# Kernel tuning notes

Hardware: AMD Instinct MI355X
Metric: run time of the kernel (lower is better)

## Reference

```python
import jax, jax.numpy as jnp
import numpy as np
from jax import lax


def setup_inputs() -> dict:
    key = jax.random.key(0)
    ks = jax.random.split(key, 4)
    B, Cin, H, W = 8, 64, 128, 128
    Cout, kh, kw = 64, 3, 3
    K = kh * kw
    x = jax.random.normal(ks[0], (B, Cin, H, W), jnp.float32)
    # small init so predicted offsets stay in a sensible range
    w_offset = jax.random.normal(ks[1], (2 * K, Cin, kh, kw), jnp.float32) * 0.01
    b_offset = jnp.zeros((2 * K,), jnp.float32)
    w_conv = jax.random.normal(ks[2], (Cout, Cin, kh, kw), jnp.float32) * (1.0 / np.sqrt(Cin * K))
    b_conv = jax.random.normal(ks[3], (Cout,), jnp.float32) * 0.01
    return dict(x=x, w_offset=w_offset, b_offset=b_offset, w_conv=w_conv, b_conv=b_conv)


def _deform_conv2d(x, offset, w, b, stride=(1, 1), padding=(1, 1), dilation=(1, 1)):
    B, Cin, Hin, Win = x.shape
    Cout, _, kh, kw = w.shape
    K = kh * kw
    sh, sw = stride; ph, pw = padding; dh, dw = dilation
    Hout = (Hin + 2 * ph - dh * (kh - 1) - 1) // sh + 1
    Wout = (Win + 2 * pw - dw * (kw - 1) - 1) // sw + 1
    # torchvision layout: [B, K, (dy,dx), Hout, Wout]
    off = offset.reshape(B, K, 2, Hout, Wout)
    dy, dx = off[:, :, 0], off[:, :, 1]
    hs = jnp.arange(Hout, dtype=x.dtype) * sh - ph          # [Hout]
    ws = jnp.arange(Wout, dtype=x.dtype) * sw - pw          # [Wout]
    ky = jnp.repeat(jnp.arange(kh, dtype=x.dtype) * dh, kw)  # [K]
    kx = jnp.tile(jnp.arange(kw, dtype=x.dtype) * dw, kh)    # [K]
    py = dy + (ky[:, None, None] + hs[None, :, None])[None]  # [B,K,Hout,Wout]
    px = dx + (kx[:, None, None] + ws[None, None, :])[None]

    def sample(img, py, px):
        y0 = jnp.floor(py); x0 = jnp.floor(px)
        wy1 = py - y0; wx1 = px - x0
        wy0 = 1.0 - wy1; wx0 = 1.0 - wx1

        def gather(yy, xx, wgt):
            valid = (yy >= 0) & (yy <= Hin - 1) & (xx >= 0) & (xx <= Win - 1)
            yi = jnp.clip(yy, 0, Hin - 1).astype(jnp.int32)
            xi = jnp.clip(xx, 0, Win - 1).astype(jnp.int32)
            vals = img[:, yi, xi]  # [Cin,K,Hout,Wout]
            return vals * (wgt * valid)[None]

        return (gather(y0, x0, wy0 * wx0) + gather(y0, x0 + 1, wy0 * wx1)
                + gather(y0 + 1, x0, wy1 * wx0) + gather(y0 + 1, x0 + 1, wy1 * wx1))

    sampled = jax.vmap(sample)(x, py, px)  # [B,Cin,K,Hout,Wout]
    out = jnp.einsum('bckhw,ock->bohw', sampled, w.reshape(Cout, Cin, K))
    return out + b[None, :, None, None]


def reference(x, w_offset, b_offset, w_conv, b_conv):
    # offset-predicting conv (stride 1, same padding, dilation 1)
    offset = lax.conv_general_dilated(
        x, w_offset, window_strides=(1, 1), padding=[(1, 1), (1, 1)],
        rhs_dilation=(1, 1), dimension_numbers=('NCHW', 'OIHW', 'NCHW'))
    offset = offset + b_offset[None, :, None, None]
    # deformable conv v1 (mask is None in _get_deformation)
    return _deform_conv2d(x, offset, w_conv, b_conv)
```

## Files before the change

### kernel.cpp

```cpp
#include <hip/hip_runtime.h>
#include <stdint.h>

#define H 128
#define W 128
#define CIN 64
#define COUT 64
#define NB 8
#define WR 4
#define WC 16
#define CW 20
#define PLANE 162

typedef __attribute__((ext_vector_type(4))) float f32x4;
typedef __attribute__((ext_vector_type(2))) _Float16 f16x2;
typedef __attribute__((ext_vector_type(8))) _Float16 f16x8;
typedef __attribute__((ext_vector_type(4))) unsigned int u32x4;
typedef __attribute__((ext_vector_type(2))) unsigned int u32x2;

__device__ __forceinline__ f16x2 bch2(unsigned u) { return __builtin_bit_cast(f16x2, u); }
__device__ __forceinline__ unsigned bcu(f16x2 v) { return __builtin_bit_cast(unsigned, v); }

__global__ __launch_bounds__(256) void x_to_nhwc(const float* __restrict__ x,
                                                 _Float16* __restrict__ xt) {
    __shared__ _Float16 tile[W][68];
    int bh = blockIdx.x;
    int h = bh & (H - 1), b = bh >> 7;
    int t = threadIdx.x;
    #pragma unroll
    for (int i = 0; i < 8; ++i) {
        int idx = i * 256 + t;
        int c = idx >> 5;
        int w4 = (idx & 31) << 2;
        f32x4 v = *(const f32x4*)(x + (((size_t)(b * CIN + c) * H + h) * W + w4));
        #pragma unroll
        for (int j = 0; j < 4; ++j) tile[w4 + j][c] = (_Float16)v[j];
    }
    __syncthreads();
    _Float16* dst = xt + (size_t)bh * W * CIN;
    #pragma unroll
    for (int i = 0; i < 8; ++i) {
        int idx = i * 256 + t;
        int w = idx >> 4;
        int c4 = (idx & 15) << 2;
        *(uint2*)(dst + (size_t)w * CIN + c4) = *(const uint2*)&tile[w][c4];
    }
}

__global__ __launch_bounds__(256) void prep_w(const float* __restrict__ wo,
                                              const float* __restrict__ wc,
                                              _Float16* __restrict__ wao2,
                                              _Float16* __restrict__ wac2) {
    int t = blockIdx.x * 256 + threadIdx.x;
    if (t < 18432) {
        int j = t & 7, l = (t >> 3) & 63, m = (t >> 9) & 1, kk = t >> 10;
        int cout = m * 16 + (l & 15);
        int cin = (kk & 1) * 32 + ((l >> 4) << 3) + j;
        wao2[t] = (cout < 18) ? (_Float16)wo[(cout * 64 + cin) * 9 + (kk >> 1)]
                              : (_Float16)0.f;
    } else if (t < 18432 + 36864) {
        int u = t - 18432;
        int j = u & 7, l = (u >> 3) & 63, m = (u >> 9) & 3, kk = u >> 11;
        int cout = m * 16 + (l & 15);
        int cin = (kk & 1) * 32 + ((l >> 4) << 3) + j;
        wac2[u] = (_Float16)wc[(cout * 64 + cin) * 9 + (kk >> 1)];
    }
}

__global__ __launch_bounds__(256, 4) void deform_fused(const _Float16* __restrict__ xt,
                                                       const _Float16* __restrict__ wao2,
                                                       const _Float16* __restrict__ wac2,
                                                       const float* __restrict__ bo,
                                                       const float* __restrict__ bconv,
                                                       float* __restrict__ out) {
    __shared__ u32x4   s_x[8 * PLANE];
    __shared__ unsigned s_aw[4][9][16];
    __shared__ u32x2   s_wq[4][9][16];

    int bid = blockIdx.x;
    int b = bid & 7;
    int r = bid >> 3;
    int h0 = ((r >> 3) & 31) << 2;
    int w0 = (r & 7) << 4;

    int r_lo = max(0, h0 - 2), r_hi = min(H - 1, h0 + 5);
    int c_lo = max(0, w0 - 2), c_hi = min(W - 1, w0 + WC + 1);
    int nr = r_hi - r_lo + 1, nc = c_hi - c_lo + 1;

    int t = threadIdx.x;
    int lane = t & 63, wv = t >> 6;
    int pcol = lane & 15, hq = lane >> 4;
    int h = h0 + wv;
    int wp = w0 + pcol;

    const _Float16* xb = xt + (size_t)b * H * W * CIN;

    {
        int cs = t >> 3, ch = t & 7;
        bool act = t < nc * 8;
        for (int rr = 0; rr < nr; ++rr) {
            if (act) {
                u32x4 v = *(const u32x4*)(xb + (size_t)((r_lo + rr) * W + c_lo + cs) * CIN + (ch << 3));
                s_x[ch * PLANE + rr * CW + cs] = v;
            }
        }
    }
    __syncthreads();

    f32x4 ao0 = {}, ao1 = {};
    #pragma unroll
    for (int k = 0; k < 9; ++k) {
        int yy = h + k / 3 - 1;
        int xx = wp + k % 3 - 1;
        bool valid = ((unsigned)yy < (unsigned)H) && ((unsigned)xx < (unsigned)W);
        int yc = min(max(yy, 0), H - 1);
        int xc = min(max(xx, 0), W - 1);
        int s = (yc - r_lo) * CW + (xc - c_lo);
        u32x4 ve = s_x[hq * PLANE + s];
        u32x4 vo = s_x[(4 + hq) * PLANE + s];
        u32x4 z = {};
        if (!valid) { ve = z; vo = z; }
        f16x8 be = __builtin_bit_cast(f16x8, ve);
        f16x8 bod = __builtin_bit_cast(f16x8, vo);
        const _Float16* wb = wao2 + (size_t)(4 * k) * 512 + lane * 8;
        ao0 = __builtin_amdgcn_mfma_f32_16x16x32_f16(*(const f16x8*)(wb), be, ao0, 0, 0, 0);
        ao1 = __builtin_amdgcn_mfma_f32_16x16x32_f16(*(const f16x8*)(wb + 512), be, ao1, 0, 0, 0);
        ao0 = __builtin_amdgcn_mfma_f32_16x16x32_f16(*(const f16x8*)(wb + 1024), bod, ao0, 0, 0, 0);
        ao1 = __builtin_amdgcn_mfma_f32_16x16x32_f16(*(const f16x8*)(wb + 1536), bod, ao1, 0, 0, 0);
    }

    auto setup = [&](int k, float dy, float dx) {
        float py = (float)(h + k / 3 - 1) + dy;
        float px = (float)(wp + k % 3 - 1) + dx;
        float y0f = floorf(py), x0f = floorf(px);
        float fy = py - y0f, fx = px - x0f;
        float vy0 = (y0f >= 0.f  && y0f <= 127.f) ? 1.f : 0.f;
        float vy1 = (y0f >= -1.f && y0f <= 126.f) ? 1.f : 0.f;
        float vx0 = (x0f >= 0.f  && x0f <= 127.f) ? 1.f : 0.f;
        float vx1 = (x0f >= -1.f && x0f <= 126.f) ? 1.f : 0.f;
        float g0 = (1.f - fy) * (1.f - fx) * vy0 * vx0;
        float g1 = (1.f - fy) * fx         * vy0 * vx1;
        float g2 = fy * (1.f - fx)         * vy1 * vx0;
        float g3 = fy * fx                 * vy1 * vx1;
        int y0i = (int)fminf(fmaxf(y0f, 0.f), 127.f);
        int x0i = (int)fminf(fmaxf(x0f, 0.f), 127.f);
        int y1i = (int)fminf(fmaxf(y0f + 1.f, 0.f), 127.f);
        int x1i = (int)fminf(fmaxf(x0f + 1.f, 0.f), 127.f);
        unsigned dxb = (unsigned)(x1i - x0i);
        unsigned dyb = (unsigned)(y1i - y0i);
        bool inw = (y0i >= r_lo) && (y1i <= r_hi) && (x0i >= c_lo) && (x1i <= c_hi);
        unsigned s00 = inw ? (unsigned)((y0i - r_lo) * CW + (x0i - c_lo)) : 0u;
        unsigned a00 = (unsigned)(y0i * W + x0i);
        s_aw[wv][k][pcol] = s00 | (dxb << 9) | (dyb << 10) | (inw ? 0u : (1u << 11)) | (a00 << 12);
        u32x2 wq;
        wq[0] = bcu((f16x2){(_Float16)g0, (_Float16)g1});
        wq[1] = bcu((f16x2){(_Float16)g2, (_Float16)g3});
        s_wq[wv][k][pcol] = wq;
    };
    f32x4 bo4 = *(const f32x4*)(bo + 4 * hq);
    setup(2 * hq,     ao0[0] + bo4[0], ao0[1] + bo4[1]);
    setup(2 * hq + 1, ao0[2] + bo4[2], ao0[3] + bo4[3]);
    if (hq == 0) setup(8, ao1[0] + bo[16], ao1[1] + bo[17]);
    __syncthreads();

    const _Float16* xh = xb + (hq << 3);
    const u32x4* se = s_x + hq * PLANE;
    const u32x4* so = s_x + (4 + hq) * PLANE;
    f32x4 acc[4] = {};

    unsigned AW[9];
    u32x2   WQ[9];
    #pragma unroll
    for (int k = 0; k < 9; ++k) {
        AW[k] = s_aw[wv][k][pcol];
        WQ[k] = s_wq[wv][k][pcol];
    }

    u32x4 E[2][4], O[2][4];
    #define FETCH(kk, buf)                                                    \
        {                                                                     \
            unsigned aw_ = AW[kk];                                            \
            unsigned s00_ = aw_ & 511u;                                       \
            unsigned dx_ = (aw_ >> 9) & 1u;                                   \
            unsigned dy_ = (aw_ >> 10) & 1u;                                  \
            unsigned s01_ = s00_ + dx_, s10_ = s00_ + dy_ * CW, s11_ = s10_ + dx_; \
            E[buf][0] = se[s00_]; E[buf][1] = se[s01_];                       \
            E[buf][2] = se[s10_]; E[buf][3] = se[s11_];                       \
            O[buf][0] = so[s00_]; O[buf][1] = so[s01_];                       \
            O[buf][2] = so[s10_]; O[buf][3] = so[s11_];                       \
            asm volatile("" : "+v"(E[buf][0]), "+v"(E[buf][1]),               \
                              "+v"(E[buf][2]), "+v"(E[buf][3]),               \
                              "+v"(O[buf][0]), "+v"(O[buf][1]),               \
                              "+v"(O[buf][2]), "+v"(O[buf][3]));              \
        }

    FETCH(0, 0);
    #pragma unroll
    for (int k = 0; k < 9; ++k) {
        const int cur = k & 1, nxt = cur ^ 1;
        if (k < 8) FETCH(k + 1, nxt);
        unsigned aw = AW[k];
        u32x2 wq = WQ[k];
        u32x4 e00 = E[cur][0], e01 = E[cur][1], e10 = E[cur][2], e11 = E[cur][3];
        u32x4 o00 = O[cur][0], o01 = O[cur][1], o10 = O[cur][2], o11 = O[cur][3];
        if (__builtin_expect((aw & (1u << 11)) != 0u, 0)) {
            unsigned dxb = (aw >> 9) & 1u;
            unsigned dyb = (aw >> 10) & 1u;
            unsigned a00 = aw >> 12;
            unsigned a01 = a00 + dxb;
            unsigned a10 = a00 + (dyb << 7);
            unsigned a11 = a10 + dxb;
            const _Float16* p00 = xh + (size_t)a00 * CIN;
            const _Float16* p01 = xh + (size_t)a01 * CIN;
            const _Float16* p10 = xh + (size_t)a10 * CIN;
            const _Float16* p11 = xh + (size_t)a11 * CIN;
            e00 = *(const u32x4*)p00; o00 = *(const u32x4*)(p00 + 32);
            e01 = *(const u32x4*)p01; o01 = *(const u32x4*)(p01 + 32);
            e10 = *(const u32x4*)p10; o10 = *(const u32x4*)(p10 + 32);
            e11 = *(const u32x4*)p11; o11 = *(const u32x4*)(p11 + 32);
        }
        f16x2 wab = bch2(wq[0]);
        f16x2 wcd = bch2(wq[1]);
        f16x2 w00d = (f16x2){wab[0], wab[0]};
        f16x2 w01d = (f16x2){wab[1], wab[1]};
        f16x2 w10d = (f16x2){wcd[0], wcd[0]};
        f16x2 w11d = (f16x2){wcd[1], wcd[1]};
        u32x4 fe, fo;
        #pragma unroll
        for (int d = 0; d < 4; ++d) {
            f16x2 ve = bch2(e00[d]) * w00d + bch2(e01[d]) * w01d
                     + bch2(e10[d]) * w10d + bch2(e11[d]) * w11d;
            f16x2 vo = bch2(o00[d]) * w00d + bch2(o01[d]) * w01d
                     + bch2(o10[d]) * w10d + bch2(o11[d]) * w11d;
            fe[d] = bcu(ve);
            fo[d] = bcu(vo);
        }
        f16x8 bfe = __builtin_bit_cast(f16x8, fe);
        f16x8 bfo = __builtin_bit_cast(f16x8, fo);
        const _Float16* ab = wac2 + (size_t)(8 * k) * 512 + lane * 8;
        #pragma unroll
        for (int m = 0; m < 4; ++m)
            acc[m] = __builtin_amdgcn_mfma_f32_16x16x32_f16(*(const f16x8*)(ab + m * 512), bfe, acc[m], 0, 0, 0);
        #pragma unroll
        for (int m = 0; m < 4; ++m)
            acc[m] = __builtin_amdgcn_mfma_f32_16x16x32_f16(*(const f16x8*)(ab + (4 + m) * 512), bfo, acc[m], 0, 0, 0);
    }
    #undef FETCH

    #pragma unroll
    for (int m = 0; m < 4; ++m) {
        f32x4 bc4 = *(const f32x4*)(bconv + m * 16 + (hq << 2));
        #pragma unroll
        for (int r2 = 0; r2 < 4; ++r2) {
            int co = (m << 4) + (hq << 2) + r2;
            out[(((size_t)b * COUT + co) * H + h) * W + wp] = acc[m][r2] + bc4[r2];
        }
    }
}

extern "C" void kernel_launch(void* const* d_in, const int* in_sizes, int n_in,
                              void* d_out, int out_size, void* d_ws, size_t ws_size,
                              hipStream_t stream) {
    const float* x  = (const float*)d_in[0];
    const float* wo = (const float*)d_in[1];
    const float* bo = (const float*)d_in[2];
    const float* wc = (const float*)d_in[3];
    const float* bc = (const float*)d_in[4];
    float* out = (float*)d_out;

    _Float16* xt   = (_Float16*)d_ws;
    _Float16* wao2 = (_Float16*)((char*)d_ws + (size_t)NB * H * W * CIN * 2);
    _Float16* wac2 = wao2 + 18432;

    x_to_nhwc<<<NB * H, 256, 0, stream>>>(x, xt);
    prep_w<<<(18432 + 36864 + 255) / 256, 256, 0, stream>>>(wo, wc, wao2, wac2);
    deform_fused<<<NB * H * W / (WR * WC), 256, 0, stream>>>(xt, wao2, wac2, bo, bc, out);
}
```

Before: 56.74 us.

## Split input channels across two wave halves with shared-memory reduction

Doubles the block to 512 threads. Each pair of waves splits the 64 input channels: one half handles the first 32 channels and the other the last 32, for both the offset conv and the deformable sampling plus MFMA. Partial offset sums and final accumulators are combined through shared memory with extra barriers. This halves per-thread registers and bilinear work to raise parallelism and occupancy, at the cost of duplicated offset setup reads, two reductions and more synchronisation.

```diff
diff --git a/kernel.cpp b/kernel.cpp
--- a/kernel.cpp
+++ b/kernel.cpp
@@ -10,6 +10,7 @@
 #define WC 16
 #define CW 20
 #define PLANE 162
+#define REDS 260
 
 typedef __attribute__((ext_vector_type(4))) float f32x4;
 typedef __attribute__((ext_vector_type(2))) _Float16 f16x2;
@@ -66,15 +67,14 @@
     }
 }
 
-__global__ __launch_bounds__(256, 4) void deform_fused(const _Float16* __restrict__ xt,
+__global__ __launch_bounds__(512, 5) void deform_fused(const _Float16* __restrict__ xt,
                                                        const _Float16* __restrict__ wao2,
                                                        const _Float16* __restrict__ wac2,
                                                        const float* __restrict__ bo,
                                                        const float* __restrict__ bconv,
                                                        float* __restrict__ out) {
-    __shared__ u32x4   s_x[8 * PLANE];
-    __shared__ unsigned s_aw[4][9][16];
-    __shared__ u32x2   s_wq[4][9][16];
+    __shared__ u32x4 s_x[8 * PLANE];
+    __shared__ float s_meta[4][432];
 
     int bid = blockIdx.x;
     int b = bid & 7;
@@ -88,8 +88,11 @@
 
     int t = threadIdx.x;
     int lane = t & 63, wv = t >> 6;
+    int g = wv & 3;
+    int half = wv >> 2;
     int pcol = lane & 15, hq = lane >> 4;
-    int h = h0 + wv;
+    int pl = half * 4 + hq;
+    int h = h0 + g;
     int wp = w0 + pcol;
 
     const _Float16* xb = xt + (size_t)b * H * W * CIN;
@@ -106,6 +109,8 @@
     }
     __syncthreads();
 
+    const u32x4* sp = s_x + pl * PLANE;
+
     f32x4 ao0 = {}, ao1 = {};
     #pragma unroll
     for (int k = 0; k < 9; ++k) {
@@ -115,93 +120,94 @@
         int yc = min(max(yy, 0), H - 1);
         int xc = min(max(xx, 0), W - 1);
         int s = (yc - r_lo) * CW + (xc - c_lo);
-        u32x4 ve = s_x[hq * PLANE + s];
-        u32x4 vo = s_x[(4 + hq) * PLANE + s];
+        u32x4 v = sp[s];
         u32x4 z = {};
-        if (!valid) { ve = z; vo = z; }
-        f16x8 be = __builtin_bit_cast(f16x8, ve);
-        f16x8 bod = __builtin_bit_cast(f16x8, vo);
-        const _Float16* wb = wao2 + (size_t)(4 * k) * 512 + lane * 8;
-        ao0 = __builtin_amdgcn_mfma_f32_16x16x32_f16(*(const f16x8*)(wb), be, ao0, 0, 0, 0);
-        ao1 = __builtin_amdgcn_mfma_f32_16x16x32_f16(*(const f16x8*)(wb + 512), be, ao1, 0, 0, 0);
-        ao0 = __builtin_amdgcn_mfma_f32_16x16x32_f16(*(const f16x8*)(wb + 1024), bod, ao0, 0, 0, 0);
-        ao1 = __builtin_amdgcn_mfma_f32_16x16x32_f16(*(const f16x8*)(wb + 1536), bod, ao1, 0, 0, 0);
-    }
-
-    auto setup = [&](int k, float dy, float dx) {
-        float py = (float)(h + k / 3 - 1) + dy;
-        float px = (float)(wp + k % 3 - 1) + dx;
-        float y0f = floorf(py), x0f = floorf(px);
-        float fy = py - y0f, fx = px - x0f;
-        float vy0 = (y0f >= 0.f  && y0f <= 127.f) ? 1.f : 0.f;
-        float vy1 = (y0f >= -1.f && y0f <= 126.f) ? 1.f : 0.f;
-        float vx0 = (x0f >= 0.f  && x0f <= 127.f) ? 1.f : 0.f;
-        float vx1 = (x0f >= -1.f && x0f <= 126.f) ? 1.f : 0.f;
-        float g0 = (1.f - fy) * (1.f - fx) * vy0 * vx0;
-        float g1 = (1.f - fy) * fx         * vy0 * vx1;
-        float g2 = fy * (1.f - fx)         * vy1 * vx0;
-        float g3 = fy * fx                 * vy1 * vx1;
-        int y0i = (int)fminf(fmaxf(y0f, 0.f), 127.f);
-        int x0i = (int)fminf(fmaxf(x0f, 0.f), 127.f);
-        int y1i = (int)fminf(fmaxf(y0f + 1.f, 0.f), 127.f);
-        int x1i = (int)fminf(fmaxf(x0f + 1.f, 0.f), 127.f);
-        unsigned dxb = (unsigned)(x1i - x0i);
-        unsigned dyb = (unsigned)(y1i - y0i);
-        bool inw = (y0i >= r_lo) && (y1i <= r_hi) && (x0i >= c_lo) && (x1i <= c_hi);
-        unsigned s00 = inw ? (unsigned)((y0i - r_lo) * CW + (x0i - c_lo)) : 0u;
-        unsigned a00 = (unsigned)(y0i * W + x0i);
-        s_aw[wv][k][pcol] = s00 | (dxb << 9) | (dyb << 10) | (inw ? 0u : (1u << 11)) | (a00 << 12);
-        u32x2 wq;
-        wq[0] = bcu((f16x2){(_Float16)g0, (_Float16)g1});
-        wq[1] = bcu((f16x2){(_Float16)g2, (_Float16)g3});
-        s_wq[wv][k][pcol] = wq;
-    };
-    f32x4 bo4 = *(const f32x4*)(bo + 4 * hq);
-    setup(2 * hq,     ao0[0] + bo4[0], ao0[1] + bo4[1]);
-    setup(2 * hq + 1, ao0[2] + bo4[2], ao0[3] + bo4[3]);
-    if (hq == 0) setup(8, ao1[0] + bo[16], ao1[1] + bo[17]);
-    __syncthreads();
-
-    const _Float16* xh = xb + (hq << 3);
-    const u32x4* se = s_x + hq * PLANE;
-    const u32x4* so = s_x + (4 + hq) * PLANE;
+        if (!valid) v = z;
+        f16x8 bf = __builtin_bit_cast(f16x8, v);
+        const _Float16* wb = wao2 + (size_t)(4 * k + 2 * half) * 512 + lane * 8;
+        ao0 = __builtin_amdgcn_mfma_f32_16x16x32_f16(*(const f16x8*)(wb), bf, ao0, 0, 0, 0);
+        ao1 = __builtin_amdgcn_mfma_f32_16x16x32_f16(*(const f16x8*)(wb + 512), bf, ao1, 0, 0, 0);
+    }
+
+    if (half == 1) {
+        float* sc = s_meta[g] + lane * 6;
+        sc[0] = ao0[0]; sc[1] = ao0[1]; sc[2] = ao0[2]; sc[3] = ao0[3];
+        sc[4] = ao1[0]; sc[5] = ao1[1];
+    }
+    __syncthreads();
+
+    if (half == 0) {
+        const float* sc = s_meta[g] + lane * 6;
+        float p0 = sc[0], p1 = sc[1], p2 = sc[2], p3 = sc[3], p4 = sc[4], p5 = sc[5];
+        ao0[0] += p0; ao0[1] += p1; ao0[2] += p2; ao0[3] += p3;
+        ao1[0] += p4; ao1[1] += p5;
+
+        auto setup = [&](int k, float dy, float dx) {
+            float py = (float)(h + k / 3 - 1) + dy;
+            float px = (float)(wp + k % 3 - 1) + dx;
+            float y0f = floorf(py), x0f = floorf(px);
+            float fy = py - y0f, fx = px - x0f;
+            float vy0 = (y0f >= 0.f  && y0f <= 127.f) ? 1.f : 0.f;
+            float vy1 = (y0f >= -1.f && y0f <= 126.f) ? 1.f : 0.f;
+            float vx0 = (x0f >= 0.f  && x0f <= 127.f) ? 1.f : 0.f;
+            float vx1 = (x0f >= -1.f && x0f <= 126.f) ? 1.f : 0.f;
+            float g0 = (1.f - fy) * (1.f - fx) * vy0 * vx0;
+            float g1 = (1.f - fy) * fx         * vy0 * vx1;
+            float g2 = fy * (1.f - fx)         * vy1 * vx0;
+            float g3 = fy * fx                 * vy1 * vx1;
+            int y0i = (int)fminf(fmaxf(y0f, 0.f), 127.f);
+            int x0i = (int)fminf(fmaxf(x0f, 0.f), 127.f);
+            int y1i = (int)fminf(fmaxf(y0f + 1.f, 0.f), 127.f);
+            int x1i = (int)fminf(fmaxf(x0f + 1.f, 0.f), 127.f);
+            unsigned dxb = (unsigned)(x1i - x0i);
+            unsigned dyb = (unsigned)(y1i - y0i);
+            bool inw = (y0i >= r_lo) && (y1i <= r_hi) && (x0i >= c_lo) && (x1i <= c_hi);
+            unsigned s00 = inw ? (unsigned)((y0i - r_lo) * CW + (x0i - c_lo)) : 0u;
+            unsigned a00 = (unsigned)(y0i * W + x0i);
+            unsigned awv = s00 | (dxb << 9) | (dyb << 10) | (inw ? 0u : (1u << 11)) | (a00 << 12);
+            int idx = k * 16 + pcol;
+            ((unsigned*)s_meta[g])[idx] = awv;
+            ((unsigned*)s_meta[g])[144 + 2 * idx]     = bcu((f16x2){(_Float16)g0, (_Float16)g1});
+            ((unsigned*)s_meta[g])[144 + 2 * idx + 1] = bcu((f16x2){(_Float16)g2, (_Float16)g3});
+        };
+        f32x4 bo4 = *(const f32x4*)(bo + 4 * hq);
+        setup(2 * hq,     ao0[0] + bo4[0], ao0[1] + bo4[1]);
+        setup(2 * hq + 1, ao0[2] + bo4[2], ao0[3] + bo4[3]);
+        if (hq == 0) setup(8, ao1[0] + bo[16], ao1[1] + bo[17]);
+    }
+    __syncthreads();
+
+    const _Float16* xh = xb + (pl << 3);
     f32x4 acc[4] = {};
 
     unsigned AW[9];
-    u32x2   WQ[9];
+    #pragma unroll
+    for (int k = 0; k < 9; ++k) AW[k] = ((unsigned*)s_meta[g])[k * 16 + pcol];
+
+    u32x4 C0[4], C1[4];
+    #define FETCH(kk, Cb)                                                      \
+        {                                                                      \
+            unsigned aw_ = AW[kk];                                             \
+            unsigned s00_ = aw_ & 511u;                                        \
+            unsigned dx_ = (aw_ >> 9) & 1u;                                    \
+            unsigned dy_ = (aw_ >> 10) & 1u;                                   \
+            unsigned s01_ = s00_ + dx_, s10_ = s00_ + dy_ * CW, s11_ = s10_ + dx_; \
+            Cb[0] = sp[s00_]; Cb[1] = sp[s01_];                                \
+            Cb[2] = sp[s10_]; Cb[3] = sp[s11_];                                \
+        }
+
+    FETCH(0, C0);
     #pragma unroll
     for (int k = 0; k < 9; ++k) {
-        AW[k] = s_aw[wv][k][pcol];
-        WQ[k] = s_wq[wv][k][pcol];
-    }
-
-    u32x4 E[2][4], O[2][4];
-    #define FETCH(kk, buf)                                                    \
-        {                                                                     \
-            unsigned aw_ = AW[kk];                                            \
-            unsigned s00_ = aw_ & 511u;                                       \
-            unsigned dx_ = (aw_ >> 9) & 1u;                                   \
-            unsigned dy_ = (aw_ >> 10) & 1u;                                  \
-            unsigned s01_ = s00_ + dx_, s10_ = s00_ + dy_ * CW, s11_ = s10_ + dx_; \
-            E[buf][0] = se[s00_]; E[buf][1] = se[s01_];                       \
-            E[buf][2] = se[s10_]; E[buf][3] = se[s11_];                       \
-            O[buf][0] = so[s00_]; O[buf][1] = so[s01_];                       \
-            O[buf][2] = so[s10_]; O[buf][3] = so[s11_];                       \
-            asm volatile("" : "+v"(E[buf][0]), "+v"(E[buf][1]),               \
-                              "+v"(E[buf][2]), "+v"(E[buf][3]),               \
-                              "+v"(O[buf][0]), "+v"(O[buf][1]),               \
-                              "+v"(O[buf][2]), "+v"(O[buf][3]));              \
-        }
-
-    FETCH(0, 0);
-    #pragma unroll
-    for (int k = 0; k < 9; ++k) {
-        const int cur = k & 1, nxt = cur ^ 1;
-        if (k < 8) FETCH(k + 1, nxt);
+        u32x4 c00, c01, c10, c11;
+        if (k & 1) { c00 = C1[0]; c01 = C1[1]; c10 = C1[2]; c11 = C1[3]; }
+        else       { c00 = C0[0]; c01 = C0[1]; c10 = C0[2]; c11 = C0[3]; }
+        if (k < 8) {
+            if (k & 1) { FETCH(k + 1, C0) }
+            else       { FETCH(k + 1, C1) }
+        }
         unsigned aw = AW[k];
-        u32x2 wq = WQ[k];
-        u32x4 e00 = E[cur][0], e01 = E[cur][1], e10 = E[cur][2], e11 = E[cur][3];
-        u32x4 o00 = O[cur][0], o01 = O[cur][1], o10 = O[cur][2], o11 = O[cur][3];
+        u32x2 wq = *(const u32x2*)&((unsigned*)s_meta[g])[144 + 2 * (k * 16 + pcol)];
         if (__builtin_expect((aw & (1u << 11)) != 0u, 0)) {
             unsigned dxb = (aw >> 9) & 1u;
             unsigned dyb = (aw >> 10) & 1u;
@@ -209,14 +215,10 @@
             unsigned a01 = a00 + dxb;
             unsigned a10 = a00 + (dyb << 7);
             unsigned a11 = a10 + dxb;
-            const _Float16* p00 = xh + (size_t)a00 * CIN;
-            const _Float16* p01 = xh + (size_t)a01 * CIN;
-            const _Float16* p10 = xh + (size_t)a10 * CIN;
-            const _Float16* p11 = xh + (size_t)a11 * CIN;
-            e00 = *(const u32x4*)p00; o00 = *(const u32x4*)(p00 + 32);
-            e01 = *(const u32x4*)p01; o01 = *(const u32x4*)(p01 + 32);
-            e10 = *(const u32x4*)p10; o10 = *(const u32x4*)(p10 + 32);
-            e11 = *(const u32x4*)p11; o11 = *(const u32x4*)(p11 + 32);
+            c00 = *(const u32x4*)(xh + (size_t)a00 * CIN);
+            c01 = *(const u32x4*)(xh + (size_t)a01 * CIN);
+            c10 = *(const u32x4*)(xh + (size_t)a10 * CIN);
+            c11 = *(const u32x4*)(xh + (size_t)a11 * CIN);
         }
         f16x2 wab = bch2(wq[0]);
         f16x2 wcd = bch2(wq[1]);
@@ -224,35 +226,41 @@
         f16x2 w01d = (f16x2){wab[1], wab[1]};
         f16x2 w10d = (f16x2){wcd[0], wcd[0]};
         f16x2 w11d = (f16x2){wcd[1], wcd[1]};
-        u32x4 fe, fo;
+        u32x4 fr;
         #pragma unroll
         for (int d = 0; d < 4; ++d) {
-            f16x2 ve = bch2(e00[d]) * w00d + bch2(e01[d]) * w01d
-                     + bch2(e10[d]) * w10d + bch2(e11[d]) * w11d;
-            f16x2 vo = bch2(o00[d]) * w00d + bch2(o01[d]) * w01d
-                     + bch2(o10[d]) * w10d + bch2(o11[d]) * w11d;
-            fe[d] = bcu(ve);
-            fo[d] = bcu(vo);
-        }
-        f16x8 bfe = __builtin_bit_cast(f16x8, fe);
-        f16x8 bfo = __builtin_bit_cast(f16x8, fo);
-        const _Float16* ab = wac2 + (size_t)(8 * k) * 512 + lane * 8;
+            f16x2 v = bch2(c00[d]) * w00d + bch2(c01[d]) * w01d
+                    + bch2(c10[d]) * w10d + bch2(c11[d]) * w11d;
+            fr[d] = bcu(v);
+        }
+        f16x8 bf = __builtin_bit_cast(f16x8, fr);
+        const _Float16* ab = wac2 + (size_t)(8 * k + 4 * half) * 512 + lane * 8;
         #pragma unroll
         for (int m = 0; m < 4; ++m)
-            acc[m] = __builtin_amdgcn_mfma_f32_16x16x32_f16(*(const f16x8*)(ab + m * 512), bfe, acc[m], 0, 0, 0);
+            acc[m] = __builtin_amdgcn_mfma_f32_16x16x32_f16(*(const f16x8*)(ab + m * 512), bf, acc[m], 0, 0, 0);
+    }
+    #undef FETCH
+
+    __syncthreads();
+    float* red = (float*)s_x;
+    if (half == 0) {
         #pragma unroll
         for (int m = 0; m < 4; ++m)
-            acc[m] = __builtin_amdgcn_mfma_f32_16x16x32_f16(*(const f16x8*)(ab + (4 + m) * 512), bfo, acc[m], 0, 0, 0);
-    }
-    #undef FETCH
-
-    #pragma unroll
-    for (int m = 0; m < 4; ++m) {
-        f32x4 bc4 = *(const f32x4*)(bconv + m * 16 + (hq << 2));
-        #pragma unroll
-        for (int r2 = 0; r2 < 4; ++r2) {
-            int co = (m << 4) + (hq << 2) + r2;
-            out[(((size_t)b * COUT + co) * H + h) * W + wp] = acc[m][r2] + bc4[r2];
+            #pragma unroll
+            for (int r2 = 0; r2 < 4; ++r2)
+                red[(m * 4 + r2) * REDS + g * 64 + lane] = acc[m][r2];
+    }
+    __syncthreads();
+    if (half == 1) {
+        #pragma unroll
+        for (int m = 0; m < 4; ++m) {
+            f32x4 bc4 = *(const f32x4*)(bconv + m * 16 + (hq << 2));
+            #pragma unroll
+            for (int r2 = 0; r2 < 4; ++r2) {
+                int co = (m << 4) + (hq << 2) + r2;
+                float v = acc[m][r2] + red[(m * 4 + r2) * REDS + g * 64 + lane] + bc4[r2];
+                out[(((size_t)b * COUT + co) * H + h) * W + wp] = v;
+            }
         }
     }
 }
@@ -273,5 +281,5 @@
 
     x_to_nhwc<<<NB * H, 256, 0, stream>>>(x, xt);
     prep_w<<<(18432 + 36864 + 255) / 256, 256, 0, stream>>>(wo, wc, wao2, wac2);
-    deform_fused<<<NB * H * W / (WR * WC), 256, 0, stream>>>(xt, wao2, wac2, bo, bc, out);
-}
+    deform_fused<<<NB * H * W / (WR * WC), 512, 0, stream>>>(xt, wao2, wac2, bo, bc, out);
+}
```

Result: faster. 54.74 us (-3.5%).
